# Kernel optimization log

Measured on AMD Instinct MI355X. Metric: run time of the kernel, lower is better.

The kernel has to match this reference:

```python
import jax, jax.numpy as jnp
import numpy as np

B, N, K = 4, 4096, 16      # batch, points, knn neighbors (knn_point(16, ...))
CIN, C = 9, 128            # in_channels = 3 + extra(6); block width
NCLS = 13


def setup_inputs():
    key = jax.random.key(0)
    ks = jax.random.split(key, 16)
    def w(i, shape):
        return jax.random.normal(ks[i], shape, jnp.float32) * 0.05
    return {
        "inputs": jax.random.normal(ks[0], (B, CIN, N), jnp.float32),
        "emb_w1": w(1, (C, CIN)),
        "emb_s1": jnp.ones((C,), jnp.float32),
        "emb_b1": jnp.zeros((C,), jnp.float32),
        "emb_w2": w(2, (C, C)),
        "emb_s2": jnp.ones((C,), jnp.float32),
        "emb_b2": jnp.zeros((C,), jnp.float32),
        "blk_wq": w(3, (3, C, C)),
        "blk_wk": w(4, (3, C, C)),
        "blk_wv": w(5, (3, C, C)),
        "blk_wpos": w(6, (3, C, 3)),
        "blk_wo": w(7, (3, C, C)),
        "blk_s": jnp.ones((3, C), jnp.float32),
        "blk_b": jnp.zeros((3, C), jnp.float32),
        "fuse_w": w(8, (1024, 3 * C)),
        "fuse_s": jnp.ones((1024,), jnp.float32),
        "fuse_b": jnp.zeros((1024,), jnp.float32),
        "cls_w1": w(9, (512, 3072)),
        "cls_bias1": jnp.zeros((512,), jnp.float32),
        "cls_s1": jnp.ones((512,), jnp.float32),
        "cls_sh1": jnp.zeros((512,), jnp.float32),
        "cls_w2": w(10, (256, 512)),
        "cls_bias2": jnp.zeros((256,), jnp.float32),
        "cls_s2": jnp.ones((256,), jnp.float32),
        "cls_sh2": jnp.zeros((256,), jnp.float32),
        "cls_w3": w(11, (NCLS, 256)),
        "cls_bias3": jnp.zeros((NCLS,), jnp.float32),
    }


def reference(inputs, emb_w1, emb_s1, emb_b1, emb_w2, emb_s2, emb_b2,
              blk_wq, blk_wk, blk_wv, blk_wpos, blk_wo, blk_s, blk_b,
              fuse_w, fuse_s, fuse_b,
              cls_w1, cls_bias1, cls_s1, cls_sh1,
              cls_w2, cls_bias2, cls_s2, cls_sh2,
              cls_w3, cls_bias3):
    xyz = inputs[:, :3, :]                                    # [B,3,N]
    # --- brute-force 16-NN (knn_point): pairwise sq. distances + top-k ---
    sq = jnp.sum(xyz * xyz, axis=1)                           # [B,N]
    d = sq[:, :, None] + sq[:, None, :] - 2.0 * jnp.einsum('bcn,bcm->bnm', xyz, xyz)
    _, idx = jax.lax.top_k(-d, K)                             # [B,N,K] nearest (self incl.)
    gather = jax.vmap(lambda t, i: t[i])                      # [N,c],[N,K] -> [N,K,c]

    def cbr(x, w, s, b):                                      # Conv1d(1x1,no bias)+BN(eval)+ReLU
        return jax.nn.relu(s[None, :, None] * jnp.einsum('oc,bcn->bon', w, x) + b[None, :, None])

    x = cbr(cbr(inputs, emb_w1, emb_s1, emb_b1), emb_w2, emb_s2, emb_b2)  # [B,C,N]

    xyz_t = jnp.transpose(xyz, (0, 2, 1))                     # [B,N,3]
    rel = xyz_t[:, :, None, :] - gather(xyz_t, idx)           # [B,N,K,3] relative coords
    scale = 1.0 / jnp.sqrt(jnp.asarray(C, jnp.float32))

    xs = []
    for i in range(3):                                        # PVDSA_Res blocks (point-branch local attention)
        q = jnp.einsum('oc,bcn->bno', blk_wq[i], x)           # [B,N,C]
        k = jnp.einsum('oc,bcn->bno', blk_wk[i], x)
        v = jnp.einsum('oc,bcn->bno', blk_wv[i], x)
        k_n = gather(k, idx)                                  # [B,N,K,C]
        v_n = gather(v, idx) + jnp.einsum('oc,bnkc->bnko', blk_wpos[i], rel)
        attn = jax.nn.softmax(jnp.einsum('bnc,bnkc->bnk', q, k_n) * scale, axis=-1)
        agg = jnp.einsum('bnk,bnkc->bnc', attn, v_n)
        y = jnp.einsum('oc,bnc->bon', blk_wo[i], agg)         # out projection -> [B,C,N]
        x = x + jax.nn.relu(blk_s[i][None, :, None] * y + blk_b[i][None, :, None])  # res=True
        xs.append(x)

    x = jnp.concatenate(xs, axis=1)                           # [B,3C,N]
    x = fuse_s[None, :, None] * jnp.einsum('oc,bcn->bon', fuse_w, x) + fuse_b[None, :, None]
    x = jnp.where(x > 0, x, 0.2 * x)                          # LeakyReLU(0.2) -> [B,1024,N]

    g = jnp.concatenate([jnp.max(x, axis=-1), jnp.mean(x, axis=-1)], axis=1)  # [B,2048]
    b_, _, n_ = x.shape
    x = jnp.concatenate([x, jnp.broadcast_to(g[:, :, None], (b_, g.shape[1], n_))], axis=1)  # [B,3072,N]

    def cbbr(x, w, bias, s, sh):                              # Conv1d(1x1,bias)+BN(eval)+ReLU
        return jax.nn.relu(s[None, :, None] * (jnp.einsum('oc,bcn->bon', w, x) + bias[None, :, None]) + sh[None, :, None])

    x = cbbr(x, cls_w1, cls_bias1, cls_s1, cls_sh1)           # Dropout = identity (eval)
    x = cbbr(x, cls_w2, cls_bias2, cls_s2, cls_sh2)
    return jnp.einsum('oc,bcn->bon', cls_w3, x) + cls_bias3[None, :, None]  # [B,NCLS,N]
```

## Files before the change

### kernel.cpp

```cpp
#include <hip/hip_runtime.h>


#define NB 4
#define NP 4096
#define NT 16384

#define SCRATCH_BYTES (132u*1024u*1024u)
__device__ __align__(256) unsigned char g_scratch[SCRATCH_BYTES];

typedef __attribute__((ext_vector_type(8))) short short8;
typedef __attribute__((ext_vector_type(4))) float f32x4;
typedef __attribute__((ext_vector_type(4))) unsigned short ushort4v;

__device__ __forceinline__ float bf2f(unsigned short u){
  unsigned int v = ((unsigned int)u) << 16;
  return __builtin_bit_cast(float, v);
}
__device__ __forceinline__ unsigned short f2bf(float f){
  unsigned int x = __builtin_bit_cast(unsigned int, f);
  x += 0x7fffu + ((x >> 16) & 1u);
  return (unsigned short)(x >> 16);
}
__device__ __forceinline__ float sq3(float x, float y, float z){
  return __fadd_rn(__fadd_rn(__fmul_rn(x,x), __fmul_rn(y,y)), __fmul_rn(z,z));
}

#define KINS4(a0,a1,a2,a3,dd) do{ float _d=(dd);\
  a3=fminf(fmaxf(a2,_d),a3); a2=fminf(fmaxf(a1,_d),a2);\
  a1=fminf(fmaxf(a0,_d),a1); a0=fminf(a0,_d);}while(0)

#define KDECLD float d0=3.0e38f,d1=3.0e38f,d2=3.0e38f,d3=3.0e38f,d4=3.0e38f,\
  d5=3.0e38f,d6=3.0e38f,d7=3.0e38f,d8=3.0e38f,d9=3.0e38f,d10=3.0e38f,\
  d11=3.0e38f,d12=3.0e38f,d13=3.0e38f,d14=3.0e38f,d15=3.0e38f
#define KINSD(dd) do{ float _d=(dd); \
  d15=fminf(fmaxf(d14,_d),d15); d14=fminf(fmaxf(d13,_d),d14); \
  d13=fminf(fmaxf(d12,_d),d13); d12=fminf(fmaxf(d11,_d),d12); \
  d11=fminf(fmaxf(d10,_d),d11); d10=fminf(fmaxf(d9 ,_d),d10); \
  d9 =fminf(fmaxf(d8 ,_d),d9 ); d8 =fminf(fmaxf(d7 ,_d),d8 ); \
  d7 =fminf(fmaxf(d6 ,_d),d7 ); d6 =fminf(fmaxf(d5 ,_d),d6 ); \
  d5 =fminf(fmaxf(d4 ,_d),d5 ); d4 =fminf(fmaxf(d3 ,_d),d4 ); \
  d3 =fminf(fmaxf(d2 ,_d),d3 ); d2 =fminf(fmaxf(d1 ,_d),d2 ); \
  d1 =fminf(fmaxf(d0 ,_d),d1 ); d0 =fminf(d0,_d); }while(0)

#define KDECL KDECLD; int i0=0,i1=0,i2=0,i3=0,i4=0,i5=0,i6=0,i7=0,i8=0,\
  i9=0,i10=0,i11=0,i12=0,i13=0,i14=0,i15=0
#define KINS(dd,mm) do{ float _d=(dd); int _m=(mm); \
  bool c15 = _d < d15; \
  bool c14 = _d < d14;  i15 = c14 ? i14 : (c15 ? _m : i15);  d15 = fminf(fmaxf(d14,_d), d15); \
  bool c13 = _d < d13;  i14 = c13 ? i13 : (c14 ? _m : i14);  d14 = fminf(fmaxf(d13,_d), d14); \
  bool c12 = _d < d12;  i13 = c12 ? i12 : (c13 ? _m : i13);  d13 = fminf(fmaxf(d12,_d), d13); \
  bool c11 = _d < d11;  i12 = c11 ? i11 : (c12 ? _m : i12);  d12 = fminf(fmaxf(d11,_d), d12); \
  bool c10 = _d < d10;  i11 = c10 ? i10 : (c11 ? _m : i11);  d11 = fminf(fmaxf(d10,_d), d11); \
  bool c9  = _d < d9;   i10 = c9  ? i9  : (c10 ? _m : i10);  d10 = fminf(fmaxf(d9 ,_d), d10); \
  bool c8  = _d < d8;   i9  = c8  ? i8  : (c9  ? _m : i9 );  d9  = fminf(fmaxf(d8 ,_d), d9 ); \
  bool c7  = _d < d7;   i8  = c7  ? i7  : (c8  ? _m : i8 );  d8  = fminf(fmaxf(d7 ,_d), d8 ); \
  bool c6  = _d < d6;   i7  = c6  ? i6  : (c7  ? _m : i7 );  d7  = fminf(fmaxf(d6 ,_d), d7 ); \
  bool c5  = _d < d5;   i6  = c5  ? i5  : (c6  ? _m : i6 );  d6  = fminf(fmaxf(d5 ,_d), d6 ); \
  bool c4  = _d < d4;   i5  = c4  ? i4  : (c5  ? _m : i5 );  d5  = fminf(fmaxf(d4 ,_d), d5 ); \
  bool c3  = _d < d3;   i4  = c3  ? i3  : (c4  ? _m : i4 );  d4  = fminf(fmaxf(d3 ,_d), d4 ); \
  bool c2  = _d < d2;   i3  = c2  ? i2  : (c3  ? _m : i3 );  d3  = fminf(fmaxf(d2 ,_d), d3 ); \
  bool c1  = _d < d1;   i2  = c1  ? i1  : (c2  ? _m : i2 );  d2  = fminf(fmaxf(d1 ,_d), d2 ); \
  bool c0  = _d < d0;   i1  = c0  ? i0  : (c1  ? _m : i1 );  d1  = fminf(fmaxf(d0 ,_d), d1 ); \
  i0 = c0 ? _m : i0;  d0 = fminf(d0,_d); }while(0)

struct CvtArgs {
  const float* src[8];
  unsigned dstOff[8];
  int n[8];
};
__global__ __launch_bounds__(256) void cvt_all(CvtArgs a)
{
  int y = blockIdx.y;
  const float* src = a.src[y];
  unsigned short* dst = (unsigned short*)(g_scratch + a.dstOff[y]);
  int n = a.n[y];
  if (y == 7){
    for (int i = blockIdx.x*256 + threadIdx.x; i < n; i += gridDim.x*256){
      int r = i >> 10, c = i & 1023;
      dst[i] = f2bf(src[(size_t)r*3072 + c]);
    }
  } else {
    for (int i = blockIdx.x*256 + threadIdx.x; i < n; i += gridDim.x*256)
      dst[i] = f2bf(src[i]);
  }
}

__global__ __launch_bounds__(256) void knn_p1(const float* __restrict__ in,
                                              unsigned pdOff)
{
  float* pdist = (float*)(g_scratch + pdOff);
  __shared__ float4 sp[256];
  int b = blockIdx.z, qc = blockIdx.x, cc = blockIdx.y;
  const float* xb = in + (size_t)b*9*NP;
  int base = cc*256;
  {
    int i = threadIdx.x;
    float x = xb[base+i], y = xb[NP+base+i], z = xb[2*NP+base+i];
    sp[i] = make_float4(x,y,z, x*x+y*y+z*z);
  }
  __syncthreads();
  int n = qc*256 + threadIdx.x;
  float xn=xb[n], yn=xb[NP+n], zn=xb[2*NP+n];
  float sqn = xn*xn + yn*yn + zn*zn;
  float A0=3e38f,A1=3e38f,A2=3e38f,A3=3e38f;
  float B0=3e38f,B1=3e38f,B2=3e38f,B3=3e38f;
  float C0=3e38f,C1=3e38f,C2=3e38f,C3=3e38f;
  float D0=3e38f,D1=3e38f,D2=3e38f,D3=3e38f;
  for (int mm=0; mm<256; mm+=4){
    float4 p0 = sp[mm], p1 = sp[mm+1], p2 = sp[mm+2], p3 = sp[mm+3];
    float e0 = sqn + p0.w - 2.f*(xn*p0.x + yn*p0.y + zn*p0.z);
    float e1 = sqn + p1.w - 2.f*(xn*p1.x + yn*p1.y + zn*p1.z);
    float e2 = sqn + p2.w - 2.f*(xn*p2.x + yn*p2.y + zn*p2.z);
    float e3 = sqn + p3.w - 2.f*(xn*p3.x + yn*p3.y + zn*p3.z);
    KINS4(A0,A1,A2,A3,e0);
    KINS4(B0,B1,B2,B3,e1);
    KINS4(C0,C1,C2,C3,e2);
    KINS4(D0,D1,D2,D3,e3);
  }
  size_t ob = ((size_t)(b*16+cc)*16)*NP + n;
  pdist[ob+ 0*(size_t)NP]=A0; pdist[ob+ 1*(size_t)NP]=A1; pdist[ob+ 2*(size_t)NP]=A2; pdist[ob+ 3*(size_t)NP]=A3;
  pdist[ob+ 4*(size_t)NP]=B0; pdist[ob+ 5*(size_t)NP]=B1; pdist[ob+ 6*(size_t)NP]=B2; pdist[ob+ 7*(size_t)NP]=B3;
  pdist[ob+ 8*(size_t)NP]=C0; pdist[ob+ 9*(size_t)NP]=C1; pdist[ob+10*(size_t)NP]=C2; pdist[ob+11*(size_t)NP]=C3;
  pdist[ob+12*(size_t)NP]=D0; pdist[ob+13*(size_t)NP]=D1; pdist[ob+14*(size_t)NP]=D2; pdist[ob+15*(size_t)NP]=D3;
}

__global__ __launch_bounds__(256) void knn_thr(unsigned pdOff, unsigned thrOff)
{
  const float* pdist = (const float*)(g_scratch + pdOff);
  float* thr = (float*)(g_scratch + thrOff);
  int t = blockIdx.x*256 + threadIdx.x;
  int b = t >> 12, n = t & 4095;
  KDECLD;
  for (int cc=0; cc<16; ++cc){
    size_t ob = ((size_t)(b*16+cc)*16)*NP + n;
    #pragma unroll
    for (int j=0;j<16;j++){ KINSD(pdist[ob + (size_t)j*NP]); }
  }
  thr[t] = d15*1.000002f + 2e-4f;
}

__global__ __launch_bounds__(256) void knn_p2(const float* __restrict__ in,
                                              unsigned thrOff, unsigned pdOff, unsigned piOff)
{
  const float* thr = (const float*)(g_scratch + thrOff);
  float* pdist = (float*)(g_scratch + pdOff);
  int*   pidx  = (int*)  (g_scratch + piOff);
  __shared__ float4 sp[256];
  int b = blockIdx.z, qc = blockIdx.x, cc = blockIdx.y;
  const float* xb = in + (size_t)b*9*NP;
  int base = cc*256;
  {
    int i = threadIdx.x;
    float x = xb[base+i], y = xb[NP+base+i], z = xb[2*NP+base+i];
    sp[i] = make_float4(x,y,z,sq3(x,y,z));
  }
  __syncthreads();
  int n = qc*256 + threadIdx.x;
  float xn=xb[n], yn=xb[NP+n], zn=xb[2*NP+n];
  float sqn = sq3(xn,yn,zn);
  float th = thr[(b<<12) + n];
  size_t o = ((size_t)((b*16 + cc)*NP + n))*16;
  int cnt = 0;
  for (int mm=0; mm<256; ++mm){
    float4 p = sp[mm];
    float dot = __fadd_rn(__fadd_rn(__fmul_rn(xn,p.x), __fmul_rn(yn,p.y)), __fmul_rn(zn,p.z));
    float d = __fsub_rn(__fadd_rn(sqn, p.w), __fmul_rn(2.0f, dot));
    if (d <= th && cnt < 16){
      pdist[o+cnt] = d;
      pidx[o+cnt] = base + mm;
      cnt++;
    }
  }
  if (cnt < 16) pdist[o+cnt] = 3.0e38f;
}

__global__ __launch_bounds__(64) void knn_mrg(unsigned pdOff, unsigned piOff, unsigned idxOff)
{
  const float* pdist = (const float*)(g_scratch + pdOff);
  const int*   pidx  = (const int*)  (g_scratch + piOff);
  int*         idxOut= (int*)(g_scratch + idxOff);
  int t = blockIdx.x*64 + threadIdx.x;
  int b = t >> 12, n = t & 4095;
  KDECL;
  for (int cc=0; cc<16; ++cc){
    size_t o = ((size_t)((b*16 + cc)*NP + n))*16;
    #pragma unroll 1
    for (int j=0;j<16;j++){
      float pd = pdist[o+j];
      if (pd >= 1.0e38f) break;
      KINS(pd, pidx[o+j]);
    }
  }
  idxOut[t*16+ 0]=i0;  idxOut[t*16+ 1]=i1;  idxOut[t*16+ 2]=i2;  idxOut[t*16+ 3]=i3;
  idxOut[t*16+ 4]=i4;  idxOut[t*16+ 5]=i5;  idxOut[t*16+ 6]=i6;  idxOut[t*16+ 7]=i7;
  idxOut[t*16+ 8]=i8;  idxOut[t*16+ 9]=i9;  idxOut[t*16+10]=i10; idxOut[t*16+11]=i11;
  idxOut[t*16+12]=i12; idxOut[t*16+13]=i13; idxOut[t*16+14]=i14; idxOut[t*16+15]=i15;
}

__global__ __launch_bounds__(256) void emb1_kernel(const float* __restrict__ in,
                                                   const float* __restrict__ w1,
                                                   const float* __restrict__ s1,
                                                   const float* __restrict__ b1,
                                                   unsigned x1Off)
{
  unsigned short* x1 = (unsigned short*)(g_scratch + x1Off);
  int og = blockIdx.y*32;
  __shared__ float wf[32*9], sf[32], bf_[32];
  for (int i = threadIdx.x; i < 32*9; i += 256) wf[i] = w1[og*9 + i];
  if (threadIdx.x < 32){ sf[threadIdx.x]=s1[og+threadIdx.x]; bf_[threadIdx.x]=b1[og+threadIdx.x]; }
  __syncthreads();
  int t = blockIdx.x*256 + threadIdx.x;
  int b = t >> 12, n = t & 4095;
  float v[9];
  #pragma unroll
  for (int c=0;c<9;c++) v[c] = in[((size_t)b*9 + c)*NP + n];
  for (int o=0;o<32;o+=2){
    float a0=0.f, a1=0.f;
    #pragma unroll
    for (int c=0;c<9;c++){ a0 += wf[o*9+c]*v[c]; a1 += wf[(o+1)*9+c]*v[c]; }
    a0 = fmaxf(sf[o]*a0 + bf_[o], 0.f);
    a1 = fmaxf(sf[o+1]*a1 + bf_[o+1], 0.f);
    unsigned pk = (unsigned)f2bf(a0) | ((unsigned)f2bf(a1) << 16);
    *(unsigned*)(x1 + (size_t)t*128 + og + o) = pk;
  }
}

enum { EPI_PLAIN=0, EPI_RELU_SB=1, EPI_RES=2, EPI_LEAKY=3, EPI_CLS=4 };

template<int EPI, bool EXB>
__device__ __forceinline__ void gemm_body(
    int M0, int T0,
    const unsigned short* W, const unsigned short* X, unsigned short* out,
    int Xstride, int Xoff, int outStride, int outOff,
    const float* sPtr, const float* bPtr,
    const float* extraIn, unsigned extraOffB, int extraStride,
    unsigned resOffB, int resStride, int resOff,
    int K, int Astride, int lane)
{
  int r = lane & 15, q = lane >> 4;
  f32x4 acc[4][4];
  #pragma unroll
  for (int i=0;i<4;i++)
    #pragma unroll
    for (int j=0;j<4;j++)
      #pragma unroll
      for (int u=0;u<4;u++) acc[i][j][u] = 0.f;

  const unsigned short* Arow[4]; const unsigned short* Brow[4];
  #pragma unroll
  for (int i=0;i<4;i++) Arow[i] = W + (size_t)(M0 + i*16 + r)*Astride + q*8;
  #pragma unroll
  for (int j=0;j<4;j++) Brow[j] = X + (size_t)(T0 + j*16 + r)*Xstride + Xoff + q*8;

  for (int k0=0; k0<K; k0+=32){
    short8 a[4], bfr[4];
    #pragma unroll
    for (int i=0;i<4;i++) a[i]   = *(const short8*)(Arow[i] + k0);
    #pragma unroll
    for (int j=0;j<4;j++) bfr[j] = *(const short8*)(Brow[j] + k0);
    #pragma unroll
    for (int i=0;i<4;i++)
      #pragma unroll
      for (int j=0;j<4;j++)
        acc[i][j] = __builtin_amdgcn_mfma_f32_16x16x32_bf16(a[i], bfr[j], acc[i][j], 0, 0, 0);
  }

  #pragma unroll
  for (int i=0;i<4;i++){
    int m = M0 + i*16 + q*4;
    float sv[4], bv[4];
    if constexpr (EPI != EPI_PLAIN){
      #pragma unroll
      for (int u=0;u<4;u++){ sv[u]=sPtr[m+u]; bv[u]=bPtr[m+u]; }
    }
    #pragma unroll
    for (int j=0;j<4;j++){
      int token = T0 + j*16 + r;
      float ex[4];
      if constexpr (EPI == EPI_CLS){
        int bb = token >> 12;
        #pragma unroll
        for (int u=0;u<4;u++)
          ex[u] = EXB ? extraIn[bb*extraStride + m + u]
                      : ((const float*)(g_scratch + extraOffB))[bb*extraStride + m + u];
      }
      float resv[4];
      if constexpr (EPI == EPI_RES){
        const unsigned short* resPtr = (const unsigned short*)(g_scratch + resOffB);
        ushort4v rv = *(const ushort4v*)(resPtr + (size_t)token*resStride + resOff + m);
        #pragma unroll
        for (int u=0;u<4;u++) resv[u]=bf2f(rv[u]);
      }
      ushort4v ov;
      #pragma unroll
      for (int u=0;u<4;u++){
        float a = acc[i][j][u];
        float vo;
        if constexpr (EPI == EPI_PLAIN)        vo = a;
        else if constexpr (EPI == EPI_RELU_SB) vo = fmaxf(sv[u]*a + bv[u], 0.f);
        else if constexpr (EPI == EPI_RES)     vo = resv[u] + fmaxf(sv[u]*a + bv[u], 0.f);
        else if constexpr (EPI == EPI_LEAKY){  float tt = sv[u]*a + bv[u]; vo = tt>0.f ? tt : 0.2f*tt; }
        else { vo = fmaxf(sv[u]*(a + ex[u]) + bv[u], 0.f); }
        ov[u] = f2bf(vo);
      }
      *(ushort4v*)(out + (size_t)token*outStride + outOff + m) = ov;
    }
  }
}

template<int EPI, bool EXB>
__global__ __launch_bounds__(256) void gemm_tok(
    unsigned W0off, unsigned W1off, unsigned W2off,
    unsigned O0off, unsigned O1off, unsigned O2off,
    unsigned XoffB, int Xstride, int Xoff,
    int outStride, int outOff,
    const float* sPtr, const float* bPtr,
    const float* extraIn, unsigned extraOffB, int extraStride,
    unsigned resOffB, int resStride, int resOff,
    int K, int Astride)
{
  const unsigned short* X = (const unsigned short*)(g_scratch + XoffB);
  unsigned wOffB   = (blockIdx.z==0) ? W0off : ((blockIdx.z==1) ? W1off : W2off);
  unsigned outOffB = (blockIdx.z==0) ? O0off : ((blockIdx.z==1) ? O1off : O2off);
  const unsigned short* W = (const unsigned short*)(g_scratch + wOffB);
  unsigned short* out = (unsigned short*)(g_scratch + outOffB);
  int lane = threadIdx.x & 63, wave = threadIdx.x >> 6;
  int M0 = blockIdx.x*128 + (wave>>1)*64;
  int T0 = blockIdx.y*128 + (wave&1)*64;
  gemm_body<EPI,EXB>(M0, T0, W, X, out, Xstride, Xoff, outStride, outOff,
                     sPtr, bPtr, extraIn, extraOffB, extraStride,
                     resOffB, resStride, resOff, K, Astride, lane);
}

template<int EPI, bool EXB>
__global__ __launch_bounds__(128) void gemm_small(
    unsigned W0off, unsigned W1off, unsigned W2off,
    unsigned O0off, unsigned O1off, unsigned O2off,
    unsigned XoffB, int Xstride, int Xoff,
    int outStride, int outOff,
    const float* sPtr, const float* bPtr,
    const float* extraIn, unsigned extraOffB, int extraStride,
    unsigned resOffB, int resStride, int resOff,
    int K, int Astride)
{
  const unsigned short* X = (const unsigned short*)(g_scratch + XoffB);
  unsigned wOffB   = (blockIdx.z==0) ? W0off : ((blockIdx.z==1) ? W1off : W2off);
  unsigned outOffB = (blockIdx.z==0) ? O0off : ((blockIdx.z==1) ? O1off : O2off);
  const unsigned short* W = (const unsigned short*)(g_scratch + wOffB);
  unsigned short* out = (unsigned short*)(g_scratch + outOffB);
  int lane = threadIdx.x & 63, wave = threadIdx.x >> 6;
  int M0 = blockIdx.x*64;
  int T0 = blockIdx.y*128 + wave*64;
  gemm_body<EPI,EXB>(M0, T0, W, X, out, Xstride, Xoff, outStride, outOff,
                     sPtr, bPtr, extraIn, extraOffB, extraStride,
                     resOffB, resStride, resOff, K, Astride, lane);
}

__global__ __launch_bounds__(256) void attn_kernel(
  unsigned qOff, unsigned kOff, unsigned vOff, unsigned idxOff,
  const float* __restrict__ in, const float* __restrict__ wpos,
  unsigned aggOff)
{
  const unsigned short* Q  = (const unsigned short*)(g_scratch + qOff);
  const unsigned short* Kf = (const unsigned short*)(g_scratch + kOff);
  const unsigned short* V  = (const unsigned short*)(g_scratch + vOff);
  const int* idx           = (const int*)(g_scratch + idxOff);
  unsigned short* agg      = (unsigned short*)(g_scratch + aggOff);

  int lane = threadIdx.x & 63, wv = threadIdx.x >> 6;
  int t = blockIdx.x*4 + wv;
  int b = t >> 12, n = t & 4095;
  const float* xb = in + (size_t)b*9*NP;
  int c0 = lane*2;

  unsigned qv = *(const unsigned*)(Q + (size_t)t*128 + c0);
  float q0 = bf2f((unsigned short)(qv & 0xffff)), q1 = bf2f((unsigned short)(qv >> 16));
  float xn = xb[n], yn = xb[NP+n], zn = xb[2*NP+n];
  float wp00=wpos[c0*3+0],     wp01=wpos[c0*3+1],     wp02=wpos[c0*3+2];
  float wp10=wpos[(c0+1)*3+0], wp11=wpos[(c0+1)*3+1], wp12=wpos[(c0+1)*3+2];

  int mi[16]; float s[16];
  #pragma unroll
  for (int j=0;j<16;j++) mi[j] = idx[(size_t)t*16 + j] & 4095;
  #pragma unroll
  for (int j=0;j<16;j++){
    unsigned kv = *(const unsigned*)(Kf + ((size_t)(b<<12) + mi[j])*128 + c0);
    float p = q0*bf2f((unsigned short)(kv & 0xffff)) + q1*bf2f((unsigned short)(kv >> 16));
    #pragma unroll
    for (int o=32;o>=1;o>>=1) p += __shfl_xor(p, o, 64);
    s[j] = p;
  }
  const float scale = 0.08838834764831845f;
  float mx = s[0];
  #pragma unroll
  for (int j=1;j<16;j++) mx = fmaxf(mx, s[j]);
  float e[16], sum = 0.f;
  #pragma unroll
  for (int j=0;j<16;j++){ e[j] = __expf((s[j]-mx)*scale); sum += e[j]; }
  float inv = 1.f / sum;

  float a0=0.f, a1=0.f;
  #pragma unroll
  for (int j=0;j<16;j++){
    int m = mi[j];
    float w = e[j]*inv;
    unsigned vv = *(const unsigned*)(V + ((size_t)(b<<12) + m)*128 + c0);
    float rx = xn - xb[m];
    float ry = yn - xb[NP+m];
    float rz = zn - xb[2*NP+m];
    float p0 = wp00*rx + wp01*ry + wp02*rz;
    float p1 = wp10*rx + wp11*ry + wp12*rz;
    a0 += w*(bf2f((unsigned short)(vv & 0xffff)) + p0);
    a1 += w*(bf2f((unsigned short)(vv >> 16)) + p1);
  }
  unsigned pk = (unsigned)f2bf(a0) | ((unsigned)f2bf(a1) << 16);
  *(unsigned*)(agg + (size_t)t*128 + c0) = pk;
}

__global__ __launch_bounds__(256) void pool_part(unsigned xfOff, unsigned gpOff)
{
  const unsigned short* xf = (const unsigned short*)(g_scratch + xfOff);
  float* gp = (float*)(g_scratch + gpOff);
  int b = blockIdx.x >> 7, cblk = (blockIdx.x >> 3) & 15, seg = blockIdx.x & 7;
  int cl = threadIdx.x & 63, tg = threadIdx.x >> 6;
  int c = cblk*64 + cl;
  float mx = -3.0e38f, sm = 0.f;
  for (int n = seg*512 + tg; n < (seg+1)*512; n += 4){
    float v = bf2f(xf[((size_t)(b<<12) + n)*1024 + c]);
    mx = fmaxf(mx, v); sm += v;
  }
  __shared__ float smx[4][64], ssm[4][64];
  smx[tg][cl]=mx; ssm[tg][cl]=sm;
  __syncthreads();
  if (tg==0){
    #pragma unroll
    for (int k=1;k<4;k++){ mx = fmaxf(mx, smx[k][cl]); sm += ssm[k][cl]; }
    gp[((b*8 + seg)*2 + 0)*1024 + c] = mx;
    gp[((b*8 + seg)*2 + 1)*1024 + c] = sm;
  }
}
__global__ __launch_bounds__(256) void pool_final(unsigned gpOff, unsigned gOff)
{
  const float* gp = (const float*)(g_scratch + gpOff);
  float* g = (float*)(g_scratch + gOff);
  int b = blockIdx.x;
  for (int c = threadIdx.x; c < 1024; c += 256){
    float mx = -3.0e38f, sm = 0.f;
    #pragma unroll
    for (int seg=0; seg<8; ++seg){
      mx = fmaxf(mx, gp[((b*8 + seg)*2 + 0)*1024 + c]);
      sm += gp[((b*8 + seg)*2 + 1)*1024 + c];
    }
    g[b*2048 + c] = mx;
    g[b*2048 + 1024 + c] = sm * (1.f/4096.f);
  }
}

__global__ __launch_bounds__(256) void gterm_kernel(const float* __restrict__ w1,
                                                    const float* __restrict__ bias1,
                                                    unsigned gOff, unsigned gbOff)
{
  const float* g = (const float*)(g_scratch + gOff);
  float* gb = (float*)(g_scratch + gbOff);
  int b = blockIdx.x >> 3, og = (blockIdx.x & 7)*64;
  int ol = threadIdx.x & 63, cq = threadIdx.x >> 6;
  int o = og + ol;
  const float* wrow = w1 + (size_t)o*3072 + 1024 + cq*512;
  const float* gp = g + b*2048 + cq*512;
  float acc = 0.f;
  for (int c=0;c<512;c+=4){
    float4 wv4 = *(const float4*)(wrow + c);
    acc += wv4.x*gp[c] + wv4.y*gp[c+1] + wv4.z*gp[c+2] + wv4.w*gp[c+3];
  }
  __shared__ float sred[4][64];
  sred[cq][ol] = acc;
  __syncthreads();
  if (cq==0){
    acc += sred[1][ol] + sred[2][ol] + sred[3][ol];
    gb[b*512 + o] = acc + bias1[o];
  }
}

__global__ __launch_bounds__(256) void cls3_kernel(unsigned c2Off,
                                                   const float* __restrict__ w3,
                                                   const float* __restrict__ bias3,
                                                   float* __restrict__ outp)
{
  const unsigned short* c2 = (const unsigned short*)(g_scratch + c2Off);
  __shared__ float wf[13*256];
  __shared__ float bf3[13];
  for (int i=threadIdx.x;i<13*256;i+=256) wf[i]=w3[i];
  if (threadIdx.x < 13) bf3[threadIdx.x]=bias3[threadIdx.x];
  __syncthreads();
  int lane = threadIdx.x & 63, wv = threadIdx.x >> 6;
  int tl = lane >> 2, cq = lane & 3;
  int t = blockIdx.x*64 + wv*16 + tl;
  const unsigned short* xrow = c2 + (size_t)t*256 + cq*64;
  float acc[13];
  #pragma unroll
  for (int o=0;o<13;o++) acc[o]=0.f;
  for (int c=0;c<64;c+=8){
    short8 xv = *(const short8*)(xrow + c);
    float xs[8];
    #pragma unroll
    for (int u=0;u<8;u++) xs[u]=bf2f((unsigned short)xv[u]);
    #pragma unroll
    for (int o=0;o<13;o++){
      const float* wr = wf + o*256 + cq*64 + c;
      #pragma unroll
      for (int u=0;u<8;u++) acc[o] += wr[u]*xs[u];
    }
  }
  #pragma unroll
  for (int o=0;o<13;o++){
    acc[o] += __shfl_xor(acc[o], 1, 64);
    acc[o] += __shfl_xor(acc[o], 2, 64);
  }
  if (cq==0){
    int b = t >> 12, n = t & 4095;
    #pragma unroll
    for (int o=0;o<13;o++)
      outp[((size_t)b*13 + o)*NP + n] = acc[o] + bf3[o];
  }
}

extern "C" void kernel_launch(void* const* d_in, const int* in_sizes, int n_in,
                              void* d_out, int out_size, void* d_ws, size_t ws_size,
                              hipStream_t stream) {
  (void)in_sizes; (void)n_in; (void)out_size; (void)d_ws; (void)ws_size;
  const float* in      = (const float*)d_in[0];
  const float* emb_w1  = (const float*)d_in[1];
  const float* emb_s1  = (const float*)d_in[2];
  const float* emb_b1  = (const float*)d_in[3];
  const float* emb_w2  = (const float*)d_in[4];
  const float* emb_s2  = (const float*)d_in[5];
  const float* emb_b2  = (const float*)d_in[6];
  const float* blk_wq  = (const float*)d_in[7];
  const float* blk_wk  = (const float*)d_in[8];
  const float* blk_wv  = (const float*)d_in[9];
  const float* blk_wpos= (const float*)d_in[10];
  const float* blk_wo  = (const float*)d_in[11];
  const float* blk_s   = (const float*)d_in[12];
  const float* blk_b   = (const float*)d_in[13];
  const float* fuse_w  = (const float*)d_in[14];
  const float* fuse_s  = (const float*)d_in[15];
  const float* fuse_b  = (const float*)d_in[16];
  const float* cls_w1  = (const float*)d_in[17];
  const float* cls_b1  = (const float*)d_in[18];
  const float* cls_s1  = (const float*)d_in[19];
  const float* cls_sh1 = (const float*)d_in[20];
  const float* cls_w2  = (const float*)d_in[21];
  const float* cls_b2  = (const float*)d_in[22];
  const float* cls_s2  = (const float*)d_in[23];
  const float* cls_sh2 = (const float*)d_in[24];
  const float* cls_w3  = (const float*)d_in[25];
  const float* cls_b3  = (const float*)d_in[26];

  const unsigned MB = 1u<<20, KB = 1024u;
  const unsigned OFF_IDX   = 0;
  const unsigned OFF_WQ    = 1*MB;
  const unsigned OFF_WK    = 1*MB + 128*KB;
  const unsigned OFF_WV    = 1*MB + 256*KB;
  const unsigned OFF_WO    = 1*MB + 384*KB;
  const unsigned OFF_WEMB2 = 1*MB + 512*KB;
  const unsigned OFF_WFUSE = 1*MB + 576*KB;
  const unsigned OFF_WW1   = 3*MB;
  const unsigned OFF_WW2   = 4*MB;
  const unsigned OFF_X1    = 5*MB;
  const unsigned OFF_X0    = 9*MB;
  const unsigned OFF_XCAT  = 13*MB;
  const unsigned OFF_QB    = 25*MB;
  const unsigned OFF_KB    = 29*MB;
  const unsigned OFF_VB    = 33*MB;
  const unsigned OFF_AGG   = 37*MB;
  const unsigned OFF_XF    = 41*MB;
  const unsigned OFF_C1    = 73*MB;
  const unsigned OFF_C2    = 89*MB;
  const unsigned OFF_G     = 97*MB;
  const unsigned OFF_GB    = 97*MB + 64*KB;
  const unsigned OFF_GP    = 97*MB + 128*KB;
  const unsigned OFF_THR   = 97*MB + 512*KB;
  const unsigned OFF_PD    = 98*MB;
  const unsigned OFF_PI    = 114*MB;
  float* outp = (float*)d_out;

  CvtArgs ca;
  ca.src[0]=emb_w2;  ca.dstOff[0]=OFF_WEMB2; ca.n[0]=128*128;
  ca.src[1]=blk_wq;  ca.dstOff[1]=OFF_WQ;    ca.n[1]=3*128*128;
  ca.src[2]=blk_wk;  ca.dstOff[2]=OFF_WK;    ca.n[2]=3*128*128;
  ca.src[3]=blk_wv;  ca.dstOff[3]=OFF_WV;    ca.n[3]=3*128*128;
  ca.src[4]=blk_wo;  ca.dstOff[4]=OFF_WO;    ca.n[4]=3*128*128;
  ca.src[5]=fuse_w;  ca.dstOff[5]=OFF_WFUSE; ca.n[5]=1024*384;
  ca.src[6]=cls_w2;  ca.dstOff[6]=OFF_WW2;   ca.n[6]=256*512;
  ca.src[7]=cls_w1;  ca.dstOff[7]=OFF_WW1;   ca.n[7]=512*1024;
  cvt_all<<<dim3(64,8), 256, 0, stream>>>(ca);

  knn_p1<<<dim3(16,16,4), 256, 0, stream>>>(in, OFF_PD);
  knn_thr<<<dim3(64), 256, 0, stream>>>(OFF_PD, OFF_THR);
  knn_p2<<<dim3(16,16,4), 256, 0, stream>>>(in, OFF_THR, OFF_PD, OFF_PI);
  knn_mrg<<<dim3(256), 64, 0, stream>>>(OFF_PD, OFF_PI, OFF_IDX);
  emb1_kernel<<<dim3(64,4), 256, 0, stream>>>(in, emb_w1, emb_s1, emb_b1, OFF_X1);
  gemm_small<EPI_RELU_SB,false><<<dim3(2,128,1), 128, 0, stream>>>(
      OFF_WEMB2, OFF_WEMB2, OFF_WEMB2, OFF_X0, OFF_X0, OFF_X0,
      OFF_X1, 128, 0, 128, 0, emb_s2, emb_b2,
      nullptr, 0, 0, 0, 0, 0, 128, 128);
  for (int i=0;i<3;i++){
    unsigned wq = OFF_WQ + i*32768, wk = OFF_WK + i*32768;
    unsigned wv = OFF_WV + i*32768, wo = OFF_WO + i*32768;
    const float* wp = blk_wpos + i*128*3;
    const float* si = blk_s + i*128;
    const float* bi = blk_b + i*128;
    unsigned XiOff = (i==0) ? OFF_X0 : OFF_XCAT;
    int Xs = (i==0) ? 128 : 384;
    int Xo = (i==0) ? 0 : (i-1)*128;
    gemm_small<EPI_PLAIN,false><<<dim3(2,128,3), 128, 0, stream>>>(
        wq, wk, wv, OFF_QB, OFF_KB, OFF_VB,
        XiOff, Xs, Xo, 128, 0, nullptr, nullptr,
        nullptr, 0, 0, 0, 0, 0, 128, 128);
    attn_kernel<<<dim3(4096), 256, 0, stream>>>(OFF_QB, OFF_KB, OFF_VB, OFF_IDX, in, wp, OFF_AGG);
    gemm_small<EPI_RES,false><<<dim3(2,128,1), 128, 0, stream>>>(
        wo, wo, wo, OFF_XCAT, OFF_XCAT, OFF_XCAT,
        OFF_AGG, 128, 0, 384, i*128, si, bi,
        nullptr, 0, 0, XiOff, Xs, Xo, 128, 128);
  }
  gemm_tok<EPI_LEAKY,false><<<dim3(8,128,1), 256, 0, stream>>>(
      OFF_WFUSE, OFF_WFUSE, OFF_WFUSE, OFF_XF, OFF_XF, OFF_XF,
      OFF_XCAT, 384, 0, 1024, 0, fuse_s, fuse_b,
      nullptr, 0, 0, 0, 0, 0, 384, 384);
  pool_part<<<dim3(512), 256, 0, stream>>>(OFF_XF, OFF_GP);
  pool_final<<<dim3(4), 256, 0, stream>>>(OFF_GP, OFF_G);
  gterm_kernel<<<dim3(32), 256, 0, stream>>>(cls_w1, cls_b1, OFF_G, OFF_GB);
  gemm_tok<EPI_CLS,false><<<dim3(4,128,1), 256, 0, stream>>>(
      OFF_WW1, OFF_WW1, OFF_WW1, OFF_C1, OFF_C1, OFF_C1,
      OFF_XF, 1024, 0, 512, 0, cls_s1, cls_sh1,
      nullptr, OFF_GB, 512, 0, 0, 0, 1024, 1024);
  gemm_small<EPI_CLS,true><<<dim3(4,128,1), 128, 0, stream>>>(
      OFF_WW2, OFF_WW2, OFF_WW2, OFF_C2, OFF_C2, OFF_C2,
      OFF_C1, 512, 0, 256, 0, cls_s2, cls_sh2,
      cls_b2, 0, 0, 0, 0, 0, 512, 512);
  cls3_kernel<<<dim3(256), 256, 0, stream>>>(OFF_C2, cls_w3, cls_b3, outp);
}
```

Measured before the change: 610.5 us.

## Prefetch next K-slice into registers and swizzle GEMM block order for XCD locality

The token-major MFMA GEMM body now loads the next 32-wide K slice of A and B into registers before issuing the MFMAs for the current slice. This overlaps global-load latency with matrix math, at the cost of extra VGPRs. The gemm_tok kernel also remaps its linear block index so that blocks landing on the same XCD (lin&7) share contiguous token tiles, aiming for better L2 reuse of the X operand. The remap assumes the grid has 128 token blocks in y.

```diff
diff --git a/kernel.cpp b/kernel.cpp
--- a/kernel.cpp
+++ b/kernel.cpp
@@ -252,18 +252,32 @@
   #pragma unroll
   for (int j=0;j<4;j++) Brow[j] = X + (size_t)(T0 + j*16 + r)*Xstride + Xoff + q*8;
 
-  for (int k0=0; k0<K; k0+=32){
-    short8 a[4], bfr[4];
-    #pragma unroll
-    for (int i=0;i<4;i++) a[i]   = *(const short8*)(Arow[i] + k0);
-    #pragma unroll
-    for (int j=0;j<4;j++) bfr[j] = *(const short8*)(Brow[j] + k0);
+  short8 a[4], bfr[4];
+  #pragma unroll
+  for (int i=0;i<4;i++) a[i]   = *(const short8*)(Arow[i]);
+  #pragma unroll
+  for (int j=0;j<4;j++) bfr[j] = *(const short8*)(Brow[j]);
+  for (int k0=32; k0<K; k0+=32){
+    short8 a2[4], b2[4];
+    #pragma unroll
+    for (int i=0;i<4;i++) a2[i] = *(const short8*)(Arow[i] + k0);
+    #pragma unroll
+    for (int j=0;j<4;j++) b2[j] = *(const short8*)(Brow[j] + k0);
     #pragma unroll
     for (int i=0;i<4;i++)
       #pragma unroll
       for (int j=0;j<4;j++)
         acc[i][j] = __builtin_amdgcn_mfma_f32_16x16x32_bf16(a[i], bfr[j], acc[i][j], 0, 0, 0);
-  }
+    #pragma unroll
+    for (int i=0;i<4;i++) a[i] = a2[i];
+    #pragma unroll
+    for (int j=0;j<4;j++) bfr[j] = b2[j];
+  }
+  #pragma unroll
+  for (int i=0;i<4;i++)
+    #pragma unroll
+    for (int j=0;j<4;j++)
+      acc[i][j] = __builtin_amdgcn_mfma_f32_16x16x32_bf16(a[i], bfr[j], acc[i][j], 0, 0, 0);
 
   #pragma unroll
   for (int i=0;i<4;i++){
@@ -294,13 +308,13 @@
       ushort4v ov;
       #pragma unroll
       for (int u=0;u<4;u++){
-        float a = acc[i][j][u];
+        float aa = acc[i][j][u];
         float vo;
-        if constexpr (EPI == EPI_PLAIN)        vo = a;
-        else if constexpr (EPI == EPI_RELU_SB) vo = fmaxf(sv[u]*a + bv[u], 0.f);
-        else if constexpr (EPI == EPI_RES)     vo = resv[u] + fmaxf(sv[u]*a + bv[u], 0.f);
-        else if constexpr (EPI == EPI_LEAKY){  float tt = sv[u]*a + bv[u]; vo = tt>0.f ? tt : 0.2f*tt; }
-        else { vo = fmaxf(sv[u]*(a + ex[u]) + bv[u], 0.f); }
+        if constexpr (EPI == EPI_PLAIN)        vo = aa;
+        else if constexpr (EPI == EPI_RELU_SB) vo = fmaxf(sv[u]*aa + bv[u], 0.f);
+        else if constexpr (EPI == EPI_RES)     vo = resv[u] + fmaxf(sv[u]*aa + bv[u], 0.f);
+        else if constexpr (EPI == EPI_LEAKY){  float tt = sv[u]*aa + bv[u]; vo = tt>0.f ? tt : 0.2f*tt; }
+        else { vo = fmaxf(sv[u]*(aa + ex[u]) + bv[u], 0.f); }
         ov[u] = f2bf(vo);
       }
       *(ushort4v*)(out + (size_t)token*outStride + outOff + m) = ov;
@@ -324,9 +338,12 @@
   unsigned outOffB = (blockIdx.z==0) ? O0off : ((blockIdx.z==1) ? O1off : O2off);
   const unsigned short* W = (const unsigned short*)(g_scratch + wOffB);
   unsigned short* out = (unsigned short*)(g_scratch + outOffB);
+  int lin = blockIdx.x + gridDim.x*blockIdx.y;
+  int bx = lin >> 7;
+  int by = (lin & 7)*16 + ((lin >> 3) & 15);
   int lane = threadIdx.x & 63, wave = threadIdx.x >> 6;
-  int M0 = blockIdx.x*128 + (wave>>1)*64;
-  int T0 = blockIdx.y*128 + (wave&1)*64;
+  int M0 = bx*128 + (wave>>1)*64;
+  int T0 = by*128 + (wave&1)*64;
   gemm_body<EPI,EXB>(M0, T0, W, X, out, Xstride, Xoff, outStride, outOff,
                      sPtr, bPtr, extraIn, extraOffB, extraStride,
                      resOffB, resStride, resOff, K, Astride, lane);
```

Result: no change. 601.7 us (-1.4%).
